# Kernel optimization log

Hardware: AMD Instinct MI355X
Metric: run time of the kernel (lower is better)

## Reference

```python
import jax, jax.numpy as jnp
import numpy as np

N_NODES = 100000
N_EDGES = 1600000
IN_DIM = 165
HIDDEN = 128
OUT_DIM = 2


def gcn_conv(x, W, b, src, dst, n_nodes):
    """PyG GCNConv: h = x @ W; add self-loops; sym-normalized scatter-add; + bias."""
    h = x @ W  # [N, F_out]
    loop = jnp.arange(n_nodes, dtype=src.dtype)
    src_f = jnp.concatenate([src, loop])  # [E + N]
    dst_f = jnp.concatenate([dst, loop])
    deg = jax.ops.segment_sum(jnp.ones(src_f.shape[0], dtype=h.dtype), dst_f,
                              num_segments=n_nodes)  # in-degree incl. self-loop
    dinv = jnp.where(deg > 0, jax.lax.rsqrt(deg), jnp.zeros_like(deg))
    norm = dinv[src_f] * dinv[dst_f]  # [E + N]
    msg = h[src_f] * norm[:, None]  # gather + scale, [E+N, F_out]
    out = jax.ops.segment_sum(msg, dst_f, num_segments=n_nodes)  # scatter-add
    return out + b


def setup_inputs() -> dict:
    key = jax.random.key(0)
    k_x, k_e, k_w1, k_b1, k_w2, k_b2 = jax.random.split(key, 6)
    x = jax.random.normal(k_x, (N_NODES, IN_DIM), dtype=jnp.float32)
    edge_index = jax.random.randint(k_e, (2, N_EDGES), 0, N_NODES, dtype=jnp.int64)
    # Glorot-like init for linear weights, zeros for bias (PyG defaults)
    W1 = jax.random.normal(k_w1, (IN_DIM, HIDDEN), dtype=jnp.float32) / np.sqrt(IN_DIM)
    b1 = jnp.zeros((HIDDEN,), dtype=jnp.float32)
    W2 = jax.random.normal(k_w2, (HIDDEN, OUT_DIM), dtype=jnp.float32) / np.sqrt(HIDDEN)
    b2 = jnp.zeros((OUT_DIM,), dtype=jnp.float32)
    return {"x": x, "edge_index": edge_index, "W1": W1, "b1": b1, "W2": W2, "b2": b2}


def reference(x, edge_index, W1, b1, W2, b2):
    src, dst = edge_index[0], edge_index[1]
    h = gcn_conv(x, W1, b1, src, dst, N_NODES)
    h = jax.nn.relu(h)
    # dropout: eval mode (training=False) -> identity
    out = gcn_conv(h, W2, b2, src, dst, N_NODES)
    return out
```

## Files before the change

kernel.cpp:

```cpp
#include <hip/hip_runtime.h>
#include <hip/hip_fp16.h>

#define N_NODES 100000
#define N_EDGES 1600000
#define IN_DIM  165
#define HIDDEN  128
#define OUT_DIM 2

#define NBKT 196
#define CHUNK 4096
#define NCHUNK ((N_EDGES + CHUNK - 1) / CHUNK)
#define PADCAP 10240
#define KPAD 176
#define GROWS 64

typedef _Float16 half8_t __attribute__((ext_vector_type(8)));
typedef _Float16 half4_t __attribute__((ext_vector_type(4)));
typedef float floatx4 __attribute__((ext_vector_type(4)));


__global__ __launch_bounds__(512) void k_part2(const int* __restrict__ src,
                                               const int* __restrict__ dst,
                                               int* __restrict__ bcnt,
                                               unsigned* __restrict__ arena) {
    __shared__ int hist[256];
    __shared__ int gbase[256];

    int t = threadIdx.x;
    int e0 = blockIdx.x * CHUNK;
    int nE = N_EDGES - e0; if (nE > CHUNK) nE = CHUNK;
    int n4 = nE >> 2;
    const int4* dst4 = (const int4*)(dst + e0);
    const int4* src4 = (const int4*)(src + e0);

    if (t < 256) hist[t] = 0;
    __syncthreads();

    for (int i = t; i < n4; i += 512) {
        int4 d = dst4[i];
        atomicAdd(&hist[d.x >> 9], 1);
        atomicAdd(&hist[d.y >> 9], 1);
        atomicAdd(&hist[d.z >> 9], 1);
        atomicAdd(&hist[d.w >> 9], 1);
    }
    __syncthreads();

    if (t < NBKT) gbase[t] = t * PADCAP + atomicAdd(&bcnt[t], hist[t]);
    if (t < 256) hist[t] = 0;
    __syncthreads();

    for (int i = t; i < n4; i += 512) {
        int4 d = dst4[i];
        int4 s = src4[i];
        #pragma unroll
        for (int j = 0; j < 4; j++) {
            int dd = (j == 0) ? d.x : (j == 1) ? d.y : (j == 2) ? d.z : d.w;
            int ss = (j == 0) ? s.x : (j == 1) ? s.y : (j == 2) ? s.z : s.w;
            int bk = dd >> 9;
            unsigned entry = (unsigned)ss | ((unsigned)(dd & 511) << 17);
            int idx = atomicAdd(&hist[bk], 1);
            arena[gbase[bk] + idx] = entry;
        }
    }
}


__global__ __launch_bounds__(1024) void k_sort4(const unsigned* __restrict__ arena,
                                                const int* __restrict__ bcnt,
                                                int* __restrict__ csr,
                                                int* __restrict__ rowstart,
                                                int* __restrict__ rowend,
                                                float* __restrict__ dinv) {
    __shared__ int cnt[512];
    __shared__ int cur[512];
    __shared__ int wsum[4];
    int b = blockIdx.x;
    int n0 = b << 9;
    int t = threadIdx.x;
    int lane = t & 63, wid = t >> 6;
    int total = bcnt[b];
    int abase = b * PADCAP;
    int dbase = b * PADCAP;
    int nt4 = total >> 2;
    const uint4* arena4 = (const uint4*)(arena + abase);

    if (t < 512) cnt[t] = 0;
    __syncthreads();
    for (int p = t; p < nt4; p += 1024) {
        uint4 e = arena4[p];
        atomicAdd(&cnt[e.x >> 17], 1);
        atomicAdd(&cnt[e.y >> 17], 1);
        atomicAdd(&cnt[e.z >> 17], 1);
        atomicAdd(&cnt[e.w >> 17], 1);
    }
    {
        int p = (nt4 << 2) + t;
        if (p < total) atomicAdd(&cnt[arena[abase + p] >> 17], 1);
    }
    __syncthreads();

    int c0 = 0, c1 = 0, s = 0, inc = 0;
    if (t < 256) {
        c0 = cnt[2 * t];
        c1 = cnt[2 * t + 1];
        s = c0 + c1;
        inc = s;
        #pragma unroll
        for (int off = 1; off < 64; off <<= 1) {
            int y = __shfl_up(inc, off);
            if (lane >= off) inc += y;
        }
        if (lane == 63) wsum[wid] = inc;
    }
    __syncthreads();
    if (t == 0) {
        int acc = 0;
        #pragma unroll
        for (int w = 0; w < 4; w++) { int tv = wsum[w]; wsum[w] = acc; acc += tv; }
    }
    __syncthreads();
    if (t < 256) {
        int base = dbase + wsum[wid] + (inc - s);
        cur[2 * t] = base;
        cur[2 * t + 1] = base + c0;
        int node0 = n0 + 2 * t;
        if (node0 < N_NODES) {
            rowstart[node0] = base;
            rowend[node0] = base + c0;
            dinv[node0] = rsqrtf((float)(c0 + 1));
        }
        if (node0 + 1 < N_NODES) {
            rowstart[node0 + 1] = base + c0;
            rowend[node0 + 1] = base + c0 + c1;
            dinv[node0 + 1] = rsqrtf((float)(c1 + 1));
        }
    }
    __syncthreads();

    for (int p = t; p < nt4; p += 1024) {
        uint4 e = arena4[p];
        #pragma unroll
        for (int j = 0; j < 4; j++) {
            unsigned entry = (j == 0) ? e.x : (j == 1) ? e.y : (j == 2) ? e.z : e.w;
            int local = (int)(entry >> 17);
            int sv = (int)(entry & 0x1FFFFu);
            int pos = atomicAdd(&cur[local], 1);
            csr[pos] = sv;
        }
    }
    {
        int p = (nt4 << 2) + t;
        if (p < total) {
            unsigned entry = arena[abase + p];
            int local = (int)(entry >> 17);
            int sv = (int)(entry & 0x1FFFFu);
            int pos = atomicAdd(&cur[local], 1);
            csr[pos] = sv;
        }
    }
}


__global__ void k_w1t(const float* __restrict__ W1, _Float16* __restrict__ w1t,
                      int* __restrict__ bcnt) {
    if (blockIdx.x == 0 && threadIdx.x < NBKT) bcnt[threadIdx.x] = 0;
    int idx = blockIdx.x * 256 + threadIdx.x;
    if (idx < HIDDEN * KPAD) {
        int c = idx / KPAD, k = idx - c * KPAD;
        float v = (k < IN_DIM) ? W1[k * HIDDEN + c] : 0.f;
        w1t[idx] = (_Float16)v;
    }
}


__global__ __launch_bounds__(256) void k_gemm1(const float* __restrict__ x,
                                               const _Float16* __restrict__ w1t,
                                               const float* __restrict__ dinv,
                                               _Float16* __restrict__ h1s) {
    __shared__ float xs[GROWS * IN_DIM];
    int t = threadIdx.x;
    int wid = t >> 6, lane = t & 63;
    int row0 = blockIdx.x * GROWS;
    int nrows = N_NODES - row0; if (nrows > GROWS) nrows = GROWS;
    int nflt = nrows * IN_DIM;

    const float4* xb4 = (const float4*)(x + (size_t)row0 * IN_DIM);
    float4* xs4 = (float4*)xs;
    int n4 = nflt >> 2;
    for (int i = t; i < n4; i += 256) xs4[i] = xb4[i];
    for (int i = (n4 << 2) + t; i < nflt; i += 256) xs[i] = x[(size_t)row0 * IN_DIM + i];
    __syncthreads();

    int mrow = wid * 16;
    if (mrow >= nrows) return;
    int m = lane & 15;
    int quad = lane >> 4;
    const float* xrow = xs + (mrow + m) * IN_DIM;
    int grow = row0 + mrow;

    floatx4 acc[8];
    #pragma unroll
    for (int i = 0; i < 8; i++) acc[i] = (floatx4)(0.f);

    #pragma unroll
    for (int kc = 0; kc < 5; kc++) {
        int kb = kc * 32 + quad * 8;
        half8_t a;
        #pragma unroll
        for (int j = 0; j < 8; j++) a[j] = (_Float16)xrow[kb + j];
        #pragma unroll
        for (int cb = 0; cb < 8; cb++) {
            int col = cb * 16 + m;
            half8_t bf = *(const half8_t*)&w1t[col * KPAD + kb];
            acc[cb] = __builtin_amdgcn_mfma_f32_16x16x32_f16(a, bf, acc[cb], 0, 0, 0);
        }
    }
    {
        int kb = 160 + quad * 4;
        half4_t a;
        #pragma unroll
        for (int j = 0; j < 4; j++)
            a[j] = (kb + j < IN_DIM) ? (_Float16)xrow[kb + j] : (_Float16)0.f;
        #pragma unroll
        for (int cb = 0; cb < 8; cb++) {
            int col = cb * 16 + m;
            half4_t bf = *(const half4_t*)&w1t[col * KPAD + kb];
            acc[cb] = __builtin_amdgcn_mfma_f32_16x16x16f16(a, bf, acc[cb], 0, 0, 0);
        }
    }
    float dv[4];
    #pragma unroll
    for (int r = 0; r < 4; r++) dv[r] = dinv[grow + quad * 4 + r];
    #pragma unroll
    for (int cb = 0; cb < 8; cb++) {
        #pragma unroll
        for (int r = 0; r < 4; r++) {
            h1s[(size_t)(grow + quad * 4 + r) * HIDDEN + cb * 16 + m] =
                (_Float16)(acc[cb][r] * dv[r]);
        }
    }
}


__global__ __launch_bounds__(256) void k_agg1(const _Float16* __restrict__ h1,
                                              const int* __restrict__ rowstart,
                                              const int* __restrict__ rowend,
                                              const int* __restrict__ csr,
                                              const float* __restrict__ dinv,
                                              const float* __restrict__ b1,
                                              const float* __restrict__ W2,
                                              float2* __restrict__ h2s,
                                              int nodeoff) {
    int wid = threadIdx.x >> 6, lane = threadIdx.x & 63;
    int el = lane & 15;
    int es = lane >> 4;
    int node = nodeoff + blockIdx.x * 4 + wid;

    float acc[8];
    {
        half8_t v = *(const half8_t*)(h1 + (size_t)node * HIDDEN + el * 8);
        #pragma unroll
        for (int j = 0; j < 8; j++) acc[j] = (es == 0) ? (float)v[j] : 0.f;
    }

    int p0 = rowstart[node], p1 = rowend[node];
    int p = p0 + es;
    for (; p + 4 < p1; p += 8) {
        int sA = csr[p];
        int sB = csr[p + 4];
        half8_t vA = *(const half8_t*)(h1 + (size_t)sA * HIDDEN + el * 8);
        half8_t vB = *(const half8_t*)(h1 + (size_t)sB * HIDDEN + el * 8);
        #pragma unroll
        for (int j = 0; j < 8; j++) acc[j] += (float)vA[j];
        #pragma unroll
        for (int j = 0; j < 8; j++) acc[j] += (float)vB[j];
    }
    if (p < p1) {
        int s = csr[p];
        half8_t v = *(const half8_t*)(h1 + (size_t)s * HIDDEN + el * 8);
        #pragma unroll
        for (int j = 0; j < 8; j++) acc[j] += (float)v[j];
    }

    #pragma unroll
    for (int j = 0; j < 8; j++) {
        acc[j] += __shfl_xor(acc[j], 16);
        acc[j] += __shfl_xor(acc[j], 32);
    }

    float di = dinv[node];
    float4 bb0 = ((const float4*)b1)[el * 2];
    float4 bb1 = ((const float4*)b1)[el * 2 + 1];
    float bv[8] = {bb0.x, bb0.y, bb0.z, bb0.w, bb1.x, bb1.y, bb1.z, bb1.w};
    float a0 = 0.f, a1 = 0.f;
    #pragma unroll
    for (int j = 0; j < 8; j++) {
        float z = fmaf(di, acc[j], bv[j]);
        float r = fmaxf(z, 0.f);
        float2 w = ((const float2*)W2)[el * 8 + j];
        a0 = fmaf(r, w.x, a0);
        a1 = fmaf(r, w.y, a1);
    }
    #pragma unroll
    for (int off = 8; off; off >>= 1) {
        a0 += __shfl_xor(a0, off);
        a1 += __shfl_xor(a1, off);
    }
    if (lane == 0) h2s[node] = make_float2(di * a0, di * a1);
}


__global__ __launch_bounds__(256) void k_agg2(const float2* __restrict__ h2s,
                                              const int* __restrict__ rowstart,
                                              const int* __restrict__ rowend,
                                              const int* __restrict__ csr,
                                              const float* __restrict__ dinv,
                                              const float* __restrict__ b2,
                                              float2* __restrict__ out) {
    int wid = threadIdx.x >> 6, lane = threadIdx.x & 63;
    int sub = lane >> 4, el = lane & 15;
    int node = blockIdx.x * 16 + wid * 4 + sub;
    int p0 = rowstart[node], p1 = rowend[node];
    float ax = 0.f, ay = 0.f;
    for (int p = p0 + el; p < p1; p += 16) {
        float2 g = h2s[csr[p]];
        ax += g.x;
        ay += g.y;
    }
    #pragma unroll
    for (int off = 8; off; off >>= 1) {
        ax += __shfl_xor(ax, off);
        ay += __shfl_xor(ay, off);
    }
    if (el == 0) {
        float2 self = h2s[node];
        float di = dinv[node];
        out[node] = make_float2(fmaf(di, self.x + ax, b2[0]),
                                fmaf(di, self.y + ay, b2[1]));
    }
}


extern "C" void kernel_launch(void* const* d_in, const int* in_sizes, int n_in,
                              void* d_out, int out_size, void* d_ws, size_t ws_size,
                              hipStream_t stream) {
    const float* x  = (const float*)d_in[0];
    const int*   ei = (const int*)d_in[1];
    const float* W1 = (const float*)d_in[2];
    const float* b1 = (const float*)d_in[3];
    const float* W2 = (const float*)d_in[4];
    const float* b2 = (const float*)d_in[5];
    float* out = (float*)d_out;

    const int* src = ei;
    const int* dst = ei + N_EDGES;

    char* ws = (char*)d_ws;
    size_t off = 0;
    auto alloc = [&](size_t bytes) -> void* {
        void* p = ws + off;
        off += (bytes + 255) & ~(size_t)255;
        return p;
    };
    _Float16* h1s      = (_Float16*)alloc((size_t)N_NODES * HIDDEN * 2);
    float*    dinv     = (float*)   alloc((size_t)N_NODES * 4);
    int*      rowstart = (int*)     alloc((size_t)N_NODES * 4);
    int*      rowend   = (int*)     alloc((size_t)N_NODES * 4);
    int*      bcnt     = (int*)     alloc((size_t)NBKT * 4);
    unsigned* arena    = (unsigned*)alloc((size_t)NBKT * PADCAP * 4);
    int*      csr      = (int*)     alloc((size_t)NBKT * PADCAP * 4);
    _Float16* w1t      = (_Float16*)alloc((size_t)HIDDEN * KPAD * 2);
    float2*   h2s      = (float2*)  alloc((size_t)N_NODES * 8);

    k_w1t<<<(HIDDEN * KPAD + 255) / 256, 256, 0, stream>>>(W1, w1t, bcnt);
    k_part2<<<NCHUNK, 512, 0, stream>>>(src, dst, bcnt, arena);
    k_sort4<<<NBKT, 1024, 0, stream>>>(arena, bcnt, csr, rowstart, rowend, dinv);
    k_gemm1<<<(N_NODES + GROWS - 1) / GROWS, 256, 0, stream>>>(x, w1t, dinv, h1s);
    k_agg1<<<N_NODES / 8, 256, 0, stream>>>(h1s, rowstart, rowend, csr, dinv, b1, W2, h2s, 0);
    k_agg1<<<N_NODES / 8, 256, 0, stream>>>(h1s, rowstart, rowend, csr, dinv, b1, W2, h2s, N_NODES / 2);
    k_agg2<<<N_NODES / 16, 256, 0, stream>>>(h2s, rowstart, rowend, csr, dinv, b2, (float2*)out);
}
```

Measured before the change: 248.4 us.

## Stage x tile in LDS as padded swizzled fp16 and merge agg1 launches

The GEMM1 x tile is now converted to fp16 while it is copied into shared memory. It is stored with a 176-element row stride and an XOR swizzle, so each MFMA A fragment becomes a single vector LDS load instead of eight scalar float loads plus conversions. This halves LDS usage (about 22KB instead of 42KB) and launch bounds request 8 blocks per CU for more occupancy. The two half-sized k_agg1 launches are merged into one grid covering all nodes, which removes a launch. The staging loop now does per-element division to compute row and column, which adds ALU work.

```diff
diff --git a/kernel.cpp b/kernel.cpp
--- a/kernel.cpp
+++ b/kernel.cpp
@@ -13,6 +13,7 @@
 #define PADCAP 10240
 #define KPAD 176
 #define GROWS 64
+#define XSTRIDE 176
 
 typedef _Float16 half8_t __attribute__((ext_vector_type(8)));
 typedef _Float16 half4_t __attribute__((ext_vector_type(4)));
@@ -173,11 +174,11 @@
 }
 
 
-__global__ __launch_bounds__(256) void k_gemm1(const float* __restrict__ x,
-                                               const _Float16* __restrict__ w1t,
-                                               const float* __restrict__ dinv,
-                                               _Float16* __restrict__ h1s) {
-    __shared__ float xs[GROWS * IN_DIM];
+__global__ __launch_bounds__(256, 8) void k_gemm1(const float* __restrict__ x,
+                                                  const _Float16* __restrict__ w1t,
+                                                  const float* __restrict__ dinv,
+                                                  _Float16* __restrict__ h1s) {
+    __shared__ __align__(16) _Float16 xs[GROWS * XSTRIDE];
     int t = threadIdx.x;
     int wid = t >> 6, lane = t & 63;
     int row0 = blockIdx.x * GROWS;
@@ -185,17 +186,32 @@
     int nflt = nrows * IN_DIM;
 
     const float4* xb4 = (const float4*)(x + (size_t)row0 * IN_DIM);
-    float4* xs4 = (float4*)xs;
     int n4 = nflt >> 2;
-    for (int i = t; i < n4; i += 256) xs4[i] = xb4[i];
-    for (int i = (n4 << 2) + t; i < nflt; i += 256) xs[i] = x[(size_t)row0 * IN_DIM + i];
+    for (int i = t; i < n4; i += 256) {
+        float4 v = xb4[i];
+        int e = i << 2;
+        #pragma unroll
+        for (int j = 0; j < 4; j++) {
+            int ee = e + j;
+            int r = ee / IN_DIM;
+            int c = ee - r * IN_DIM;
+            float f = (j == 0) ? v.x : (j == 1) ? v.y : (j == 2) ? v.z : v.w;
+            xs[(r * XSTRIDE + c) ^ ((r & 7) << 3)] = (_Float16)f;
+        }
+    }
+    for (int i = t; i < GROWS * (XSTRIDE - IN_DIM); i += 256) {
+        int r = i / (XSTRIDE - IN_DIM);
+        int c = IN_DIM + (i - r * (XSTRIDE - IN_DIM));
+        xs[(r * XSTRIDE + c) ^ ((r & 7) << 3)] = (_Float16)0.f;
+    }
     __syncthreads();
 
     int mrow = wid * 16;
     if (mrow >= nrows) return;
     int m = lane & 15;
     int quad = lane >> 4;
-    const float* xrow = xs + (mrow + m) * IN_DIM;
+    int rbase = (mrow + m) * XSTRIDE;
+    int sm = (m & 7) << 3;
     int grow = row0 + mrow;
 
     floatx4 acc[8];
@@ -205,9 +221,7 @@
     #pragma unroll
     for (int kc = 0; kc < 5; kc++) {
         int kb = kc * 32 + quad * 8;
-        half8_t a;
-        #pragma unroll
-        for (int j = 0; j < 8; j++) a[j] = (_Float16)xrow[kb + j];
+        half8_t a = *(const half8_t*)&xs[(rbase + kb) ^ sm];
         #pragma unroll
         for (int cb = 0; cb < 8; cb++) {
             int col = cb * 16 + m;
@@ -217,10 +231,7 @@
     }
     {
         int kb = 160 + quad * 4;
-        half4_t a;
-        #pragma unroll
-        for (int j = 0; j < 4; j++)
-            a[j] = (kb + j < IN_DIM) ? (_Float16)xrow[kb + j] : (_Float16)0.f;
+        half4_t a = *(const half4_t*)&xs[(rbase + kb) ^ sm];
         #pragma unroll
         for (int cb = 0; cb < 8; cb++) {
             int col = cb * 16 + m;
@@ -376,7 +387,6 @@
     k_part2<<<NCHUNK, 512, 0, stream>>>(src, dst, bcnt, arena);
     k_sort4<<<NBKT, 1024, 0, stream>>>(arena, bcnt, csr, rowstart, rowend, dinv);
     k_gemm1<<<(N_NODES + GROWS - 1) / GROWS, 256, 0, stream>>>(x, w1t, dinv, h1s);
-    k_agg1<<<N_NODES / 8, 256, 0, stream>>>(h1s, rowstart, rowend, csr, dinv, b1, W2, h2s, 0);
-    k_agg1<<<N_NODES / 8, 256, 0, stream>>>(h1s, rowstart, rowend, csr, dinv, b1, W2, h2s, N_NODES / 2);
+    k_agg1<<<N_NODES / 4, 256, 0, stream>>>(h1s, rowstart, rowend, csr, dinv, b1, W2, h2s, 0);
     k_agg2<<<N_NODES / 16, 256, 0, stream>>>(h2s, rowstart, rowend, csr, dinv, b2, (float2*)out);
 }
```

New measurement: 239.4 us. 3.6% less time.
